# Performance work log

Measured on AMD Instinct MI355X. Metric: run time of the kernel, lower is better.

The kernel has to match this reference:

```python
import jax, jax.numpy as jnp
import numpy as np

NUM_BINS = 32
SIGMA_RATIO = 0.5          # Gaussian Parzen window width relative to bin spacing
SMOOTH_NR = 1e-07
SMOOTH_DR = 1e-07


def setup_inputs() -> dict:
    key = jax.random.key(0)
    k1, k2 = jax.random.split(key)
    shape = (2, 1, 96, 96, 96)
    pred = jax.random.uniform(k1, shape, dtype=jnp.float32)
    target = jax.random.uniform(k2, shape, dtype=jnp.float32)
    return {"pred": pred, "target": target}


def _parzen_weights(img_flat, bin_centers, preterm):
    # img_flat: [B, N]; bin_centers: [nb]
    # Gaussian Parzen window, normalized so each voxel's weights sum to 1 over bins.
    d = img_flat[..., None] - bin_centers          # [B, N, nb]
    w = jnp.exp(-preterm * d * d)                  # [B, N, nb]
    return w / jnp.sum(w, axis=-1, keepdims=True)


def reference(pred, target):
    B = pred.shape[0]
    nb = NUM_BINS
    bin_centers = jnp.linspace(0.0, 1.0, nb, dtype=jnp.float32)  # [nb]
    bin_width = 1.0 / (nb - 1)
    sigma = SIGMA_RATIO * bin_width
    preterm = jnp.float32(1.0 / (2.0 * sigma * sigma))

    p = pred.reshape(B, -1)    # [B, N]
    t = target.reshape(B, -1)  # [B, N]
    N = p.shape[1]

    wa = _parzen_weights(p, bin_centers, preterm)  # [B, N, nb]
    wb = _parzen_weights(t, bin_centers, preterm)  # [B, N, nb]

    # joint histogram [B, nb, nb] and marginals [B, 1, nb]
    pab = jnp.einsum('bni,bnj->bij', wa, wb) / N
    pa = jnp.mean(wa, axis=1, keepdims=True).transpose(0, 2, 1).transpose(0, 2, 1)  # [B,1,nb]
    pa = jnp.mean(wa, axis=1)[:, None, :]  # [B, 1, nb]
    pb = jnp.mean(wb, axis=1)[:, None, :]  # [B, 1, nb]

    # papb = bmm(pa^T, pb): outer product of marginals -> [B, nb, nb]
    papb = jnp.einsum('bki,bkj->bij', pa, pb)

    mi = jnp.sum(pab * jnp.log((pab + SMOOTH_NR) / (papb + SMOOTH_DR) + SMOOTH_DR),
                 axis=(-1, -2))  # [B]
    return -jnp.mean(mi)
```

## Files before the change

kernel.cpp:

```cpp
#include <hip/hip_runtime.h>
#include <hip/hip_bf16.h>

#define NBINS 32
#define CHUNK 128
#define NROWS 34
#define STR 136
#define TILE_HALVES (NROWS * STR)
#define NTHREADS 256
#define NVOX 884736
#define BPB 512
#define NSLOTS 8

typedef __attribute__((ext_vector_type(8))) _Float16 half8;
typedef __attribute__((ext_vector_type(16))) float f32x16;
typedef __attribute__((ext_vector_type(4))) int i32x4;

__device__ __forceinline__ void compute_w(float x, int& kb, _Float16* wq) {
    float tt = x * 31.0f;
    float kf = rintf(tt);
    int ki = (int)kf;
    float u = tt - kf;
    kb = ki - 3 + (u > 0.0f ? 1 : 0);
    float w[6];
    float s = 0.0f;
#pragma unroll
    for (int o = 0; o < 6; ++o) {
        int b = kb + o;
        float d = tt - (float)b;
        float e = __expf(-2.0f * d * d);
        e = ((unsigned)b < NBINS) ? e : 0.0f;
        w[o] = e;
        s += e;
    }
    float rinv = 1.0f / s;
#pragma unroll
    for (int o = 0; o < 6; ++o) wq[o] = (_Float16)(w[o] * rinv);
}

__device__ __forceinline__ void zero6(_Float16* __restrict__ L, int col, int kb) {
#pragma unroll
    for (int o = 0; o < 6; ++o) {
        int r = min(max(kb + o, -1), 32) + 1;
        L[r * STR + col] = (_Float16)0.0f;
    }
}
__device__ __forceinline__ void scatter6(_Float16* __restrict__ L, int col, int kb,
                                         const _Float16* wq) {
#pragma unroll
    for (int o = 0; o < 6; ++o) {
        int r = min(max(kb + o, -1), 32) + 1;
        L[r * STR + col] = wq[o];
    }
}

__global__ __launch_bounds__(NTHREADS, 4)
void mi_hist_kernel(const float* __restrict__ pred, const float* __restrict__ targ,
                    float* __restrict__ hist ) {
    __shared__ __attribute__((aligned(16))) _Float16 smem[4 * TILE_HALVES];

    const int tid = threadIdx.x;
    const int bx = blockIdx.x;
    const int batch = blockIdx.y;
    const int col = tid & 127;
    const bool isB = tid >= 128;
    const float* src = (isB ? targ : pred) + (size_t)batch * NVOX;
    const int toff = isB ? TILE_HALVES : 0;

    const int wid = tid >> 6;
    const int lane = tid & 63;
    const int frag = (1 + (lane & 31)) * STR + wid * 32 + 8 * (lane >> 5);

    float xs[14];
#pragma unroll
    for (int c = 0; c < 13; ++c)
        xs[c] = src[((size_t)(c * BPB + bx)) * CHUNK + col];
    const bool extra = (bx < 256);
    if (extra) xs[13] = src[((size_t)(13 * BPB + bx)) * CHUNK + col];

    {
        i32x4 z = {0, 0, 0, 0};
        i32x4* zp = (i32x4*)smem;
#pragma unroll
        for (int i = 0; i < 10; ++i) {
            int idx = i * NTHREADS + tid;
            if (idx < (4 * TILE_HALVES) / 8) zp[idx] = z;
        }
    }

    f32x16 acc;
#pragma unroll
    for (int r = 0; r < 16; ++r) acc[r] = 0.0f;

    int kbo0 = 0, kbo1 = 0;

#define DO_MFMA(BASE) { \
        const _Float16* Pp = (BASE); \
        _Pragma("unroll") \
        for (int kk = 0; kk < 2; ++kk) { \
            half8 af = *(const half8*)&Pp[frag + kk * 16]; \
            half8 bf = *(const half8*)&Pp[TILE_HALVES + frag + kk * 16]; \
            acc = __builtin_amdgcn_mfma_f32_32x32x16_f16(af, bf, acc, 0, 0, 0); \
        } }

#pragma unroll
    for (int c = 0; c < 13; ++c) {
        _Float16 wq[6];
        int kb;
        compute_w(xs[c], kb, wq);
        __syncthreads();
        _Float16* cur = smem + (c & 1) * 2 * TILE_HALVES + toff;
        if (c >= 2) zero6(cur, col, (c & 1) ? kbo1 : kbo0);
        scatter6(cur, col, kb, wq);
        if (c & 1) kbo1 = kb; else kbo0 = kb;
        if (c >= 1) DO_MFMA(smem + (((c & 1) ^ 1) * 2) * TILE_HALVES);
    }
    if (extra) {
        _Float16 wq[6];
        int kb;
        compute_w(xs[13], kb, wq);
        __syncthreads();
        _Float16* cur = smem + 2 * TILE_HALVES + toff;
        zero6(cur, col, kbo1);
        scatter6(cur, col, kb, wq);
        DO_MFMA(smem);
        __syncthreads();
        DO_MFMA(smem + 2 * TILE_HALVES);
    } else {
        __syncthreads();
        DO_MFMA(smem);
    }
    __syncthreads();

    float* red = (float*)smem;
    const int colc = lane & 31;
    const int rlo = 4 * (lane >> 5);
#pragma unroll
    for (int r = 0; r < 16; ++r) {
        int rowc = (r & 3) + 8 * (r >> 2) + rlo;
        red[wid * 1024 + rowc * 32 + colc] = acc[r];
    }
    __syncthreads();
    float* H = hist + ((size_t)(bx & (NSLOTS - 1)) * 2 + batch) * 1024;
    for (int idx = tid; idx < 1024; idx += NTHREADS) {
        float s = red[idx] + red[1024 + idx] + red[2048 + idx] + red[3072 + idx];
        atomicAdd(&H[idx], s);
    }
}

__global__ void mi_reduce_kernel(const float* __restrict__ hist, float* __restrict__ out) {
    __shared__ float s_pab[2 * NBINS * NBINS];
    __shared__ double s_pa[2][NBINS];
    __shared__ double s_pb[2][NBINS];
    __shared__ double s_red[256];
    const int tid = threadIdx.x;
    const double invN = 1.0 / (double)NVOX;

    for (int g = tid; g < 512; g += 256) {
        float4 s = make_float4(0.f, 0.f, 0.f, 0.f);
        for (int sl = 0; sl < NSLOTS; ++sl) {
            float4 v = ((const float4*)hist)[sl * 512 + g];
            s.x += v.x; s.y += v.y; s.z += v.z; s.w += v.w;
        }
        ((float4*)s_pab)[g] = s;
    }
    __syncthreads();

    if (tid < 64) {
        int b = tid >> 5, i = tid & 31;
        double s = 0.0;
        for (int j = 0; j < NBINS; ++j) s += (double)s_pab[(b * NBINS + i) * NBINS + j];
        s_pa[b][i] = s * invN;
    } else if (tid < 128) {
        int t2 = tid - 64;
        int b = t2 >> 5, j = t2 & 31;
        double s = 0.0;
        for (int i = 0; i < NBINS; ++i) s += (double)s_pab[(b * NBINS + i) * NBINS + j];
        s_pb[b][j] = s * invN;
    }
    __syncthreads();

    double acc = 0.0;
    for (int idx = tid; idx < 2 * NBINS * NBINS; idx += 256) {
        int b = idx >> 10;
        int cell = idx & 1023;
        int i = cell >> 5, j = cell & 31;
        double pab = (double)s_pab[idx] * invN;
        double papb = s_pa[b][i] * s_pb[b][j];
        acc += pab * log((pab + 1e-7) / (papb + 1e-7) + 1e-7);
    }
    s_red[tid] = acc;
    __syncthreads();
    for (int s2 = 128; s2 > 0; s2 >>= 1) {
        if (tid < s2) s_red[tid] += s_red[tid + s2];
        __syncthreads();
    }
    if (tid == 0) out[0] = (float)(-0.5 * s_red[0]);
}

extern "C" void kernel_launch(void* const* d_in, const int* in_sizes, int n_in,
                              void* d_out, int out_size, void* d_ws, size_t ws_size,
                              hipStream_t stream) {
    const float* pred = (const float*)d_in[0];
    const float* targ = (const float*)d_in[1];
    float* hist = (float*)d_ws;
    float* out = (float*)d_out;

    hipMemsetAsync(hist, 0, NSLOTS * 2 * NBINS * NBINS * sizeof(float), stream);
    dim3 grid(BPB, 2);
    hipLaunchKernelGGL(mi_hist_kernel, grid, dim3(NTHREADS), 0, stream, pred, targ, hist);
    hipLaunchKernelGGL(mi_reduce_kernel, dim3(1), dim3(256), 0, stream, hist, out);
}
```

Baseline: 31.05 us.

## Fuse final MI reduction into histogram kernel via last-block counter

Removes the separate single-block reduce kernel. A global atomic counter lets the last finishing histogram block read the slot histograms and compute the mutual information in place. Separately, the MFMA on the previous buffer is moved ahead of the zero/scatter into the current buffer, so matrix work can overlap the LDS writes. This saves one kernel launch and its gap, at the cost of a threadfence and an atomic per block, plus a serial tail on one block.

Result: slower. 96.78 us (+211.7%).

```diff
diff --git a/kernel.cpp b/kernel.cpp
--- a/kernel.cpp
+++ b/kernel.cpp
@@ -10,6 +10,7 @@
 #define NVOX 884736
 #define BPB 512
 #define NSLOTS 8
+#define NBLOCKS (2 * BPB)
 
 typedef __attribute__((ext_vector_type(8))) _Float16 half8;
 typedef __attribute__((ext_vector_type(16))) float f32x16;
@@ -55,8 +56,10 @@
 
 __global__ __launch_bounds__(NTHREADS, 4)
 void mi_hist_kernel(const float* __restrict__ pred, const float* __restrict__ targ,
-                    float* __restrict__ hist ) {
+                    float* __restrict__ hist ,
+                    int* __restrict__ counter, float* __restrict__ out) {
     __shared__ __attribute__((aligned(16))) _Float16 smem[4 * TILE_HALVES];
+    __shared__ int s_last;
 
     const int tid = threadIdx.x;
     const int bx = blockIdx.x;
@@ -108,21 +111,21 @@
         int kb;
         compute_w(xs[c], kb, wq);
         __syncthreads();
+        if (c >= 1) DO_MFMA(smem + (((c & 1) ^ 1) * 2) * TILE_HALVES);
         _Float16* cur = smem + (c & 1) * 2 * TILE_HALVES + toff;
         if (c >= 2) zero6(cur, col, (c & 1) ? kbo1 : kbo0);
         scatter6(cur, col, kb, wq);
         if (c & 1) kbo1 = kb; else kbo0 = kb;
-        if (c >= 1) DO_MFMA(smem + (((c & 1) ^ 1) * 2) * TILE_HALVES);
     }
     if (extra) {
         _Float16 wq[6];
         int kb;
         compute_w(xs[13], kb, wq);
         __syncthreads();
+        DO_MFMA(smem);
         _Float16* cur = smem + 2 * TILE_HALVES + toff;
         zero6(cur, col, kbo1);
         scatter6(cur, col, kb, wq);
-        DO_MFMA(smem);
         __syncthreads();
         DO_MFMA(smem + 2 * TILE_HALVES);
     } else {
@@ -145,23 +148,28 @@
         float s = red[idx] + red[1024 + idx] + red[2048 + idx] + red[3072 + idx];
         atomicAdd(&H[idx], s);
     }
-}
-
-__global__ void mi_reduce_kernel(const float* __restrict__ hist, float* __restrict__ out) {
-    __shared__ float s_pab[2 * NBINS * NBINS];
-    __shared__ double s_pa[2][NBINS];
-    __shared__ double s_pb[2][NBINS];
-    __shared__ double s_red[256];
-    const int tid = threadIdx.x;
+
+    __threadfence();
+    if (tid == 0) {
+        int old = __hip_atomic_fetch_add(counter, 1, __ATOMIC_ACQ_REL, __HIP_MEMORY_SCOPE_AGENT);
+        s_last = (old == NBLOCKS - 1);
+    }
+    __syncthreads();
+    if (!s_last) return;
+
+    float* s_pab = (float*)smem;
+    double* s_pa = (double*)((char*)smem + 8192);
+    double* s_pb = (double*)((char*)smem + 8704);
+    double* s_red = (double*)((char*)smem + 9216);
     const double invN = 1.0 / (double)NVOX;
 
-    for (int g = tid; g < 512; g += 256) {
-        float4 s = make_float4(0.f, 0.f, 0.f, 0.f);
-        for (int sl = 0; sl < NSLOTS; ++sl) {
-            float4 v = ((const float4*)hist)[sl * 512 + g];
-            s.x += v.x; s.y += v.y; s.z += v.z; s.w += v.w;
-        }
-        ((float4*)s_pab)[g] = s;
+    __syncthreads();
+    for (int idx = tid; idx < 2048; idx += NTHREADS) {
+        float s = 0.0f;
+        for (int sl = 0; sl < NSLOTS; ++sl)
+            s += __hip_atomic_load(&hist[sl * 2048 + idx], __ATOMIC_RELAXED,
+                                   __HIP_MEMORY_SCOPE_AGENT);
+        s_pab[idx] = s;
     }
     __syncthreads();
 
@@ -169,26 +177,26 @@
         int b = tid >> 5, i = tid & 31;
         double s = 0.0;
         for (int j = 0; j < NBINS; ++j) s += (double)s_pab[(b * NBINS + i) * NBINS + j];
-        s_pa[b][i] = s * invN;
+        s_pa[b * NBINS + i] = s * invN;
     } else if (tid < 128) {
         int t2 = tid - 64;
         int b = t2 >> 5, j = t2 & 31;
         double s = 0.0;
         for (int i = 0; i < NBINS; ++i) s += (double)s_pab[(b * NBINS + i) * NBINS + j];
-        s_pb[b][j] = s * invN;
-    }
-    __syncthreads();
-
-    double acc = 0.0;
-    for (int idx = tid; idx < 2 * NBINS * NBINS; idx += 256) {
+        s_pb[b * NBINS + j] = s * invN;
+    }
+    __syncthreads();
+
+    double accd = 0.0;
+    for (int idx = tid; idx < 2048; idx += NTHREADS) {
         int b = idx >> 10;
         int cell = idx & 1023;
         int i = cell >> 5, j = cell & 31;
         double pab = (double)s_pab[idx] * invN;
-        double papb = s_pa[b][i] * s_pb[b][j];
-        acc += pab * log((pab + 1e-7) / (papb + 1e-7) + 1e-7);
-    }
-    s_red[tid] = acc;
+        double papb = s_pa[b * NBINS + i] * s_pb[b * NBINS + j];
+        accd += pab * log((pab + 1e-7) / (papb + 1e-7) + 1e-7);
+    }
+    s_red[tid] = accd;
     __syncthreads();
     for (int s2 = 128; s2 > 0; s2 >>= 1) {
         if (tid < s2) s_red[tid] += s_red[tid + s2];
@@ -203,10 +211,11 @@
     const float* pred = (const float*)d_in[0];
     const float* targ = (const float*)d_in[1];
     float* hist = (float*)d_ws;
+    int* counter = (int*)((char*)d_ws + NSLOTS * 2048 * sizeof(float));
     float* out = (float*)d_out;
 
-    hipMemsetAsync(hist, 0, NSLOTS * 2 * NBINS * NBINS * sizeof(float), stream);
+    hipMemsetAsync(d_ws, 0, NSLOTS * 2048 * sizeof(float) + 16, stream);
     dim3 grid(BPB, 2);
-    hipLaunchKernelGGL(mi_hist_kernel, grid, dim3(NTHREADS), 0, stream, pred, targ, hist);
-    hipLaunchKernelGGL(mi_reduce_kernel, dim3(1), dim3(256), 0, stream, hist, out);
-}
+    hipLaunchKernelGGL(mi_hist_kernel, grid, dim3(NTHREADS), 0, stream,
+                       pred, targ, hist, counter, out);
+}
```

## Single-buffer LDS tiles, double the grid, and widen the reduce block

Applied to the files above, without the earlier changes.

The histogram kernel drops its double-buffered LDS tiles for a single A/B tile pair, synchronising twice per round. This halves shared-memory use and raises the launch-bounds occupancy target from 4 to 8 blocks. The grid is doubled to 1024 blocks per batch, so each block handles about 7 chunks instead of 14, and the atomic histogram slots grow to 16. The LDS row stride changes from 136 to 132 to alter bank mapping, and the final reduce kernel moves to 1024 threads. The trade is that scatter, compute and MFMA no longer overlap within a block, which relies on more resident blocks to hide latency.

Result: slower. 50.52 us (+62.7%).

```diff
diff --git a/kernel.cpp b/kernel.cpp
--- a/kernel.cpp
+++ b/kernel.cpp
@@ -4,12 +4,12 @@
 #define NBINS 32
 #define CHUNK 128
 #define NROWS 34
-#define STR 136
+#define STR 132
 #define TILE_HALVES (NROWS * STR)
 #define NTHREADS 256
 #define NVOX 884736
-#define BPB 512
-#define NSLOTS 8
+#define BPB 1024
+#define NSLOTS 16
 
 typedef __attribute__((ext_vector_type(8))) _Float16 half8;
 typedef __attribute__((ext_vector_type(16))) float f32x16;
@@ -53,10 +53,12 @@
     }
 }
 
-__global__ __launch_bounds__(NTHREADS, 4)
+__global__ __launch_bounds__(NTHREADS, 8)
 void mi_hist_kernel(const float* __restrict__ pred, const float* __restrict__ targ,
                     float* __restrict__ hist ) {
-    __shared__ __attribute__((aligned(16))) _Float16 smem[4 * TILE_HALVES];
+    __shared__ __attribute__((aligned(16))) _Float16 smem[2 * TILE_HALVES];
+    _Float16* TA = smem;
+    _Float16* TB = smem + TILE_HALVES;
 
     const int tid = threadIdx.x;
     const int bx = blockIdx.x;
@@ -64,26 +66,27 @@
     const int col = tid & 127;
     const bool isB = tid >= 128;
     const float* src = (isB ? targ : pred) + (size_t)batch * NVOX;
-    const int toff = isB ? TILE_HALVES : 0;
+    _Float16* T = isB ? TB : TA;
 
     const int wid = tid >> 6;
     const int lane = tid & 63;
     const int frag = (1 + (lane & 31)) * STR + wid * 32 + 8 * (lane >> 5);
 
-    float xs[14];
-#pragma unroll
-    for (int c = 0; c < 13; ++c)
+    const bool extra = (bx < 768);
+
+    float xs[7];
+#pragma unroll
+    for (int c = 0; c < 6; ++c)
         xs[c] = src[((size_t)(c * BPB + bx)) * CHUNK + col];
-    const bool extra = (bx < 256);
-    if (extra) xs[13] = src[((size_t)(13 * BPB + bx)) * CHUNK + col];
+    if (extra) xs[6] = src[((size_t)(6 * BPB + bx)) * CHUNK + col];
 
     {
         i32x4 z = {0, 0, 0, 0};
         i32x4* zp = (i32x4*)smem;
 #pragma unroll
-        for (int i = 0; i < 10; ++i) {
+        for (int i = 0; i < 5; ++i) {
             int idx = i * NTHREADS + tid;
-            if (idx < (4 * TILE_HALVES) / 8) zp[idx] = z;
+            if (idx < (2 * TILE_HALVES) / 8) zp[idx] = z;
         }
     }
 
@@ -91,44 +94,35 @@
 #pragma unroll
     for (int r = 0; r < 16; ++r) acc[r] = 0.0f;
 
-    int kbo0 = 0, kbo1 = 0;
-
-#define DO_MFMA(BASE) { \
-        const _Float16* Pp = (BASE); \
+    int kb_old = 0;
+
+#define DO_MFMA() { \
         _Pragma("unroll") \
         for (int kk = 0; kk < 2; ++kk) { \
-            half8 af = *(const half8*)&Pp[frag + kk * 16]; \
-            half8 bf = *(const half8*)&Pp[TILE_HALVES + frag + kk * 16]; \
+            half8 af = *(const half8*)&TA[frag + kk * 16]; \
+            half8 bf = *(const half8*)&TB[frag + kk * 16]; \
             acc = __builtin_amdgcn_mfma_f32_32x32x16_f16(af, bf, acc, 0, 0, 0); \
         } }
 
-#pragma unroll
-    for (int c = 0; c < 13; ++c) {
-        _Float16 wq[6];
-        int kb;
-        compute_w(xs[c], kb, wq);
-        __syncthreads();
-        _Float16* cur = smem + (c & 1) * 2 * TILE_HALVES + toff;
-        if (c >= 2) zero6(cur, col, (c & 1) ? kbo1 : kbo0);
-        scatter6(cur, col, kb, wq);
-        if (c & 1) kbo1 = kb; else kbo0 = kb;
-        if (c >= 1) DO_MFMA(smem + (((c & 1) ^ 1) * 2) * TILE_HALVES);
-    }
-    if (extra) {
-        _Float16 wq[6];
-        int kb;
-        compute_w(xs[13], kb, wq);
-        __syncthreads();
-        _Float16* cur = smem + 2 * TILE_HALVES + toff;
-        zero6(cur, col, kbo1);
-        scatter6(cur, col, kb, wq);
-        DO_MFMA(smem);
-        __syncthreads();
-        DO_MFMA(smem + 2 * TILE_HALVES);
-    } else {
-        __syncthreads();
-        DO_MFMA(smem);
-    }
+#define ROUND(C, ZO) { \
+        _Float16 wq[6]; int kb; \
+        compute_w(xs[C], kb, wq);         \
+        __syncthreads();                  \
+        if (ZO) zero6(T, col, kb_old);    \
+        scatter6(T, col, kb, wq); \
+        kb_old = kb; \
+        __syncthreads();                  \
+        DO_MFMA(); }
+
+    ROUND(0, false)
+    ROUND(1, true)
+    ROUND(2, true)
+    ROUND(3, true)
+    ROUND(4, true)
+    ROUND(5, true)
+    if (extra) { ROUND(6, true) }
+#undef ROUND
+
     __syncthreads();
 
     float* red = (float*)smem;
@@ -151,11 +145,11 @@
     __shared__ float s_pab[2 * NBINS * NBINS];
     __shared__ double s_pa[2][NBINS];
     __shared__ double s_pb[2][NBINS];
-    __shared__ double s_red[256];
+    __shared__ double s_red[1024];
     const int tid = threadIdx.x;
     const double invN = 1.0 / (double)NVOX;
 
-    for (int g = tid; g < 512; g += 256) {
+    for (int g = tid; g < 512; g += 1024) {
         float4 s = make_float4(0.f, 0.f, 0.f, 0.f);
         for (int sl = 0; sl < NSLOTS; ++sl) {
             float4 v = ((const float4*)hist)[sl * 512 + g];
@@ -180,7 +174,7 @@
     __syncthreads();
 
     double acc = 0.0;
-    for (int idx = tid; idx < 2 * NBINS * NBINS; idx += 256) {
+    for (int idx = tid; idx < 2 * NBINS * NBINS; idx += 1024) {
         int b = idx >> 10;
         int cell = idx & 1023;
         int i = cell >> 5, j = cell & 31;
@@ -190,7 +184,7 @@
     }
     s_red[tid] = acc;
     __syncthreads();
-    for (int s2 = 128; s2 > 0; s2 >>= 1) {
+    for (int s2 = 512; s2 > 0; s2 >>= 1) {
         if (tid < s2) s_red[tid] += s_red[tid + s2];
         __syncthreads();
     }
@@ -208,5 +202,5 @@
     hipMemsetAsync(hist, 0, NSLOTS * 2 * NBINS * NBINS * sizeof(float), stream);
     dim3 grid(BPB, 2);
     hipLaunchKernelGGL(mi_hist_kernel, grid, dim3(NTHREADS), 0, stream, pred, targ, hist);
-    hipLaunchKernelGGL(mi_reduce_kernel, dim3(1), dim3(256), 0, stream, hist, out);
-}
+    hipLaunchKernelGGL(mi_reduce_kernel, dim3(1), dim3(1024), 0, stream, hist, out);
+}
```
